# Kernel tuning notes

Hardware: AMD Instinct MI355X
Metric: run time of the kernel (lower is better)

## Reference

```python
import jax, jax.numpy as jnp
import numpy as np

B, D, K, H = 8192, 1024, 8, 2048


def setup_inputs() -> dict:
    key = jax.random.key(0)
    ks = jax.random.split(key, 4)
    x = jax.random.normal(ks[0], (B, D), dtype=jnp.float32)
    centroids = jax.random.normal(ks[1], (K, D), dtype=jnp.float32)
    W1 = jax.random.normal(ks[2], (K, D, H), dtype=jnp.float32) / np.sqrt(D).astype(np.float32)
    b1 = jnp.zeros((K, H), dtype=jnp.float32)
    W2 = jax.random.normal(ks[3], (K, H), dtype=jnp.float32) / np.sqrt(H).astype(np.float32)
    b2 = jnp.zeros((K,), dtype=jnp.float32)
    return {"x": x, "centroids": centroids, "W1": W1, "b1": b1, "W2": W2, "b2": b2}


def reference(x, centroids, W1, b1, W2, b2):
    # --- k-means hard routing: nearest centroid per sample (euclidean max_sim) ---
    # d2[b,k] = ||x_b||^2 - 2 x_b . c_k + ||c_k||^2  (avoid [B,K,D] blowup)
    d2 = (jnp.sum(x * x, axis=-1, keepdims=True)
          - 2.0 * (x @ centroids.T)
          + jnp.sum(centroids * centroids, axis=-1)[None, :])  # [B, K]
    cluster = jnp.argmin(d2, axis=-1)  # [B] int, hard assignment

    # --- per-expert log-likelihood heads (Einet stand-in), computed densely ---
    h = jnp.tanh(jnp.einsum("bd,kdh->kbh", x, W1) + b1[:, None, :])  # [K, B, H]
    lls = jnp.einsum("kbh,kh->kb", h, W2) + b2[:, None]              # [K, B]

    # --- combine: each sample takes the LL from its routed expert, original order ---
    lls_sorted = jnp.take_along_axis(lls.T, cluster[:, None], axis=1)[:, 0]  # [B]
    return lls_sorted
```

## Files before the change

kernel.cpp:

```cpp
#include <hip/hip_runtime.h>
#include <hip/hip_bf16.h>
#include <stdint.h>

#define B_N 8192
#define D_N 1024
#define K_N 8
#define H_N 2048

#define BM 320
#define BN 256
#define BK 64
#define GRID_MT 34
#define ABYTES 40960
#define BUFSZ 73728
#define RO_OFF 147456
#define PLL_OFF 148736
#define GEMM_LDS 153856

typedef unsigned int u32;
typedef unsigned short u16;
typedef __attribute__((ext_vector_type(8))) short short8;
typedef __attribute__((ext_vector_type(4))) float float4v;

struct __align__(8) us4 { u16 x, y, z, w; };

__device__ __forceinline__ u16 f2bf(float f) {
    union { float f; u32 u; } v; v.f = f;
    u32 u = v.u;
    u32 r = (u + 0x7fffu + ((u >> 16) & 1u)) >> 16;
    return (u16)r;
}

__device__ __forceinline__ float fast_tanh(float x) {
    float t = __expf(2.0f * x);
    return 1.0f - 2.0f * __builtin_amdgcn_rcpf(t + 1.0f);
}

__device__ __forceinline__ void async_copy16(void* lds, const void* g) {
    __builtin_amdgcn_global_load_lds(
        (const __attribute__((address_space(1))) void*)g,
        (__attribute__((address_space(3))) void*)lds, 16, 0, 0);
}

__global__ void prep_kernel(const float* __restrict__ w1, u16* __restrict__ w1t,
                            u32* __restrict__ counts,
                            const float* __restrict__ x, const float* __restrict__ cent,
                            const float* __restrict__ b2, u16* __restrict__ xbf,
                            int* __restrict__ cluster, float* __restrict__ out) {
    __shared__ float ts[64][65];
    int tid = threadIdx.x;
    int bid = (int)blockIdx.x;
    int m3 = bid % 3;

    if (m3 == 2) {
        int rb = bid / 3;
        int wave = tid >> 6, lane = tid & 63;
        int b = rb * 4 + wave;
        const float* xr = x + (size_t)b * D_N;

        float4 xv[4];
#pragma unroll
        for (int i = 0; i < 4; ++i)
            xv[i] = *(const float4*)(xr + i * 256 + lane * 4);

#pragma unroll
        for (int i = 0; i < 4; ++i) {
            us4 o;
            o.x = f2bf(xv[i].x); o.y = f2bf(xv[i].y);
            o.z = f2bf(xv[i].z); o.w = f2bf(xv[i].w);
            *(us4*)(xbf + (size_t)b * D_N + i * 256 + lane * 4) = o;
        }

        double acc[K_N];
#pragma unroll
        for (int k = 0; k < K_N; ++k) {
            const float* cr = cent + k * D_N;
            double s = 0.0;
#pragma unroll
            for (int i = 0; i < 4; ++i) {
                float4 cv = *(const float4*)(cr + i * 256 + lane * 4);
                double d0 = (double)xv[i].x - (double)cv.x; s += d0 * d0;
                double d1 = (double)xv[i].y - (double)cv.y; s += d1 * d1;
                double d2 = (double)xv[i].z - (double)cv.z; s += d2 * d2;
                double d3 = (double)xv[i].w - (double)cv.w; s += d3 * d3;
            }
            acc[k] = s;
        }
#pragma unroll
        for (int k = 0; k < K_N; ++k) {
            double v = acc[k];
            for (int off = 32; off; off >>= 1) v += __shfl_down(v, off);
            acc[k] = v;
        }
        if (lane == 0) {
            int best = 0; double bv = acc[0];
#pragma unroll
            for (int k = 1; k < K_N; ++k)
                if (acc[k] < bv) { bv = acc[k]; best = k; }
            cluster[b] = best;
            out[b] = b2[best];
        }
    } else {
        int wi = (bid / 3) * 2 + m3;
        if (wi == 0 && tid < K_N) counts[tid * 32] = 0;
        int hb = wi & 31, db = (wi >> 5) & 15, k = wi >> 9;
        int h0 = hb * 64, d0 = db * 64;
        const float* src = w1 + ((size_t)k * D_N + d0) * H_N + h0;
#pragma unroll
        for (int i = 0; i < 4; ++i) {
            int q = i * 256 + tid;
            int r = q >> 4, c4 = (q & 15) * 4;
            float4 v = *(const float4*)(src + (size_t)r * H_N + c4);
            ts[c4 + 0][r] = v.x; ts[c4 + 1][r] = v.y;
            ts[c4 + 2][r] = v.z; ts[c4 + 3][r] = v.w;
        }
        __syncthreads();
        u16* dst = w1t + ((size_t)k * H_N + h0) * D_N + d0;
#pragma unroll
        for (int i = 0; i < 4; ++i) {
            int q = i * 256 + tid;
            int hr = q >> 4, d4 = (q & 15) * 4;
            us4 o;
            o.x = f2bf(ts[hr][d4 + 0]); o.y = f2bf(ts[hr][d4 + 1]);
            o.z = f2bf(ts[hr][d4 + 2]); o.w = f2bf(ts[hr][d4 + 3]);
            *(us4*)(dst + (size_t)hr * D_N + d4) = o;
        }
    }
}

__global__ void scatter_kernel(const int* __restrict__ cluster,
                               u32* __restrict__ counts,
                               u32* __restrict__ idxl) {
    __shared__ u32 wcnt[4][K_N];
    __shared__ u32 gb[K_N];
    int tid = threadIdx.x;
    int b = blockIdx.x * 256 + tid;
    int lane = tid & 63, wid = tid >> 6;
    int cl = cluster[b];
    unsigned long long lower = (1ull << lane) - 1ull;
    u32 rank = 0;
#pragma unroll
    for (int k = 0; k < K_N; ++k) {
        unsigned long long mk = __ballot(cl == k);
        if (k == cl) rank = (u32)__popcll(mk & lower);
        if (lane == 0) wcnt[wid][k] = (u32)__popcll(mk);
    }
    __syncthreads();
    if (tid < K_N) {
        u32 tot = wcnt[0][tid] + wcnt[1][tid] + wcnt[2][tid] + wcnt[3][tid];
        gb[tid] = atomicAdd(&counts[tid * 32], tot);
    }
    __syncthreads();
    u32 woff = 0;
    if (wid > 0) woff += wcnt[0][cl];
    if (wid > 1) woff += wcnt[1][cl];
    if (wid > 2) woff += wcnt[2][cl];
    idxl[(size_t)cl * B_N + gb[cl] + woff + rank] = (u32)b;
}

__global__ __launch_bounds__(512, 2) void gemm_kernel(
                            const u16* __restrict__ xbf,
                            const u16* __restrict__ w1t,
                            const float* __restrict__ b1,
                            const float* __restrict__ w2,
                            const u32* __restrict__ idxl,
                            const u32* __restrict__ counts,
                            float* __restrict__ out) {
    extern __shared__ char lds[];
    int tix = (int)blockIdx.y;
    int k = -1, mt = 0, ntile = 0;
#pragma unroll
    for (int kk = 0; kk < K_N; ++kk) {
        int c = (int)counts[kk * 32];
        int t = (c + BM - 1) / BM;
        if (tix >= ntile && tix < ntile + t) { k = kk; mt = tix - ntile; }
        ntile += t;
    }
    if (k < 0) return;
    int cnt = (int)counts[k * 32];
    int nc = (int)blockIdx.x;
    int rows = cnt - mt * BM; if (rows > BM) rows = BM;
    int tid = threadIdx.x;
    int lane = tid & 63, w = tid >> 6;
    int wm = w >> 2, wn = w & 3;
    int wmbase = wm * 160;
    int h0 = nc * BN;
    int l15 = lane & 15, l4 = lane >> 4;

    u32* ro = (u32*)(lds + RO_OFF);
    float* pll = (float*)(lds + PLL_OFF);

    if (tid < BM) {
        int m = mt * BM + tid;
        int mm = m < cnt ? m : cnt - 1;
        ro[tid] = idxl[(size_t)k * B_N + mm] * (u32)(D_N * 2);
    }
    __syncthreads();

    u32 srcA[5], srcB[4];
#pragma unroll
    for (int i = 0; i < 5; ++i) {
        int c = i * 512 + tid; int r = c >> 3, j = c & 7;
        srcA[i] = ro[r] + ((u32)(j ^ (r & 7)) << 4);
    }
#pragma unroll
    for (int i = 0; i < 4; ++i) {
        int c = i * 512 + tid; int r = c >> 3, j = c & 7;
        srcB[i] = ((u32)(k * H_N + h0 + r) << 11) + ((u32)(j ^ (r & 7)) << 4);
    }
    const char* xb = (const char*)xbf;
    const char* wb = (const char*)w1t;

    int swz = l15 & 7;
    u32 aB0 = (u32)((wmbase + l15) * 128 + (((0 + l4) ^ swz) << 4));
    u32 aB1 = (u32)((wmbase + l15) * 128 + (((4 + l4) ^ swz) << 4));
    u32 bB0 = (u32)(ABYTES + (wn * 64 + l15) * 128 + (((0 + l4) ^ swz) << 4));
    u32 bB1 = (u32)(ABYTES + (wn * 64 + l15) * 128 + (((4 + l4) ^ swz) << 4));

    float4v acc[10][4];
#pragma unroll
    for (int mf = 0; mf < 10; ++mf)
#pragma unroll
        for (int nf = 0; nf < 4; ++nf)
            acc[mf][nf] = (float4v){0.f, 0.f, 0.f, 0.f};

#define STA(BUF, I, D) async_copy16((BUF) + (I) * 8192 + w * 1024, xb + srcA[I] + (D))
#define STB(BUF, I, D) async_copy16((BUF) + ABYTES + (I) * 8192 + w * 1024, wb + srcB[I] + (D))
#define BAR() do { asm volatile("" ::: "memory"); __builtin_amdgcn_s_barrier(); \
                   asm volatile("" ::: "memory"); } while (0)
#define MFMA_PHASE(MFB, BREG)                                                    \
    do {                                                                         \
        __builtin_amdgcn_s_setprio(1);                                           \
        _Pragma("unroll")                                                        \
        for (int i_ = 0; i_ < 5; ++i_) {                                         \
            if (wmbase + ((MFB) + i_) * 16 < rows) {                             \
                _Pragma("unroll")                                                \
                for (int nf_ = 0; nf_ < 4; ++nf_)                                \
                    acc[(MFB) + i_][nf_] = __builtin_amdgcn_mfma_f32_16x16x32_bf16( \
                        a[i_], BREG[nf_], acc[(MFB) + i_][nf_], 0, 0, 0);        \
            }                                                                    \
        }                                                                        \
        __builtin_amdgcn_s_setprio(0);                                           \
    } while (0)

    {
        char* Bp = lds;
        STA(Bp, 0, 0); STA(Bp, 1, 0); STA(Bp, 2, 0); STA(Bp, 3, 0); STA(Bp, 4, 0);
        STB(Bp, 0, 0); STB(Bp, 1, 0); STB(Bp, 2, 0); STB(Bp, 3, 0);
    }

    for (int t = 0; t < 16; ++t) {
        const char* Acur = lds + (t & 1) * BUFSZ;
        char* Bnx = lds + ((t + 1) & 1) * BUFSZ;
        u32 d = (u32)((t + 1) << 7);
        bool pre = (t < 15);
        short8 a[5], bC[4];

        asm volatile("s_waitcnt vmcnt(0)" ::: "memory");
        BAR();
#pragma unroll
        for (int nf = 0; nf < 4; ++nf)
            bC[nf] = *(const short8*)(Acur + bB0 + nf * 2048);
#pragma unroll
        for (int i = 0; i < 5; ++i)
            a[i] = *(const short8*)(Acur + aB0 + i * 2048);
        if (pre) { STB(Bnx, 0, d); STB(Bnx, 1, d); STB(Bnx, 2, d); }
        BAR();
        MFMA_PHASE(0, bC);

        BAR();
#pragma unroll
        for (int i = 0; i < 5; ++i)
            a[i] = *(const short8*)(Acur + aB0 + (5 + i) * 2048);
        if (pre) { STB(Bnx, 3, d); STA(Bnx, 0, d); STA(Bnx, 1, d); }
        BAR();
        MFMA_PHASE(5, bC);

        BAR();
#pragma unroll
        for (int nf = 0; nf < 4; ++nf)
            bC[nf] = *(const short8*)(Acur + bB1 + nf * 2048);
#pragma unroll
        for (int i = 0; i < 5; ++i)
            a[i] = *(const short8*)(Acur + aB1 + i * 2048);
        if (pre) { STA(Bnx, 2, d); STA(Bnx, 3, d); STA(Bnx, 4, d); }
        BAR();
        MFMA_PHASE(0, bC);

        BAR();
#pragma unroll
        for (int i = 0; i < 5; ++i)
            a[i] = *(const short8*)(Acur + aB1 + (5 + i) * 2048);
        BAR();
        MFMA_PHASE(5, bC);
    }

#undef STA
#undef STB
#undef BAR
#undef MFMA_PHASE

    float w2v[4], b1v[4];
#pragma unroll
    for (int nf = 0; nf < 4; ++nf) {
        int h = h0 + wn * 64 + nf * 16 + l15;
        w2v[nf] = w2[k * H_N + h];
        b1v[nf] = b1[k * H_N + h];
    }
#pragma unroll
    for (int mf = 0; mf < 10; ++mf) {
        float rs[4] = {0.f, 0.f, 0.f, 0.f};
#pragma unroll
        for (int nf = 0; nf < 4; ++nf) {
#pragma unroll
            for (int r = 0; r < 4; ++r)
                rs[r] += fast_tanh(acc[mf][nf][r] + b1v[nf]) * w2v[nf];
        }
#pragma unroll
        for (int r = 0; r < 4; ++r) {
            float v = rs[r];
            v += __shfl_xor(v, 8);
            v += __shfl_xor(v, 4);
            v += __shfl_xor(v, 2);
            v += __shfl_xor(v, 1);
            if (l15 == 0) pll[wn * 320 + wmbase + mf * 16 + l4 * 4 + r] = v;
        }
    }
    __syncthreads();
    if (tid < BM) {
        int m = mt * BM + tid;
        if (m < cnt) {
            u32 b = idxl[(size_t)k * B_N + m];
            atomicAdd(&out[b], pll[tid] + pll[320 + tid] + pll[640 + tid] + pll[960 + tid]);
        }
    }
}

extern "C" void kernel_launch(void* const* d_in, const int* in_sizes, int n_in,
                              void* d_out, int out_size, void* d_ws, size_t ws_size,
                              hipStream_t stream) {
    const float* x    = (const float*)d_in[0];
    const float* cent = (const float*)d_in[1];
    const float* W1   = (const float*)d_in[2];
    const float* b1   = (const float*)d_in[3];
    const float* W2   = (const float*)d_in[4];
    const float* b2   = (const float*)d_in[5];
    float* out = (float*)d_out;

    char* ws = (char*)d_ws;
    u16* xbf     = (u16*)(ws + 0);
    u16* w1t     = (u16*)(ws + 16777216);
    u32* counts  = (u32*)(ws + 50331648);
    int* cluster = (int*)(ws + 50332672);
    u32* idxl    = (u32*)(ws + 50365440);

    (void)hipFuncSetAttribute((const void*)gemm_kernel,
                              hipFuncAttributeMaxDynamicSharedMemorySize, GEMM_LDS);

    hipLaunchKernelGGL(prep_kernel, dim3(6144), dim3(256), 0, stream,
                       W1, w1t, counts, x, cent, b2, xbf, cluster, out);
    hipLaunchKernelGGL(scatter_kernel, dim3(32), dim3(256), 0, stream,
                       cluster, counts, idxl);
    hipLaunchKernelGGL(gemm_kernel, dim3(8, GRID_MT), dim3(512), GEMM_LDS, stream,
                       xbf, w1t, b1, W2, idxl, counts, out);
}
```

Before: 82.06 us.

## Shrink M tile to 256 and split K-step loads into half-stages with partial waits

Reduces the gathered-row GEMM tile from 320 to 256 rows, giving 8 MFMA row fragments per wave instead of 10 and more M tiles (grid 40). The LDS layout changes to split each 64-wide K step into two 32-wide regions with a new swizzle, and the prefetch is issued per half-stage. Waits drop from vmcnt(0) to vmcnt(4), so the second half's loads can still be in flight while the first half computes. This trades some tile-level reuse and extra tile launches for finer-grained overlap, lower register pressure and less LDS.

```diff
diff --git a/kernel.cpp b/kernel.cpp
--- a/kernel.cpp
+++ b/kernel.cpp
@@ -7,15 +7,16 @@
 #define K_N 8
 #define H_N 2048
 
-#define BM 320
+#define BM 256
 #define BN 256
 #define BK 64
-#define GRID_MT 34
-#define ABYTES 40960
-#define BUFSZ 73728
-#define RO_OFF 147456
-#define PLL_OFF 148736
-#define GEMM_LDS 153856
+#define GRID_MT 40
+#define REGB 16384
+#define BUFB 65536
+#define BOFF 32768
+#define RO_OFF 131072
+#define PLL_OFF 132096
+#define GEMM_LDS 136192
 
 typedef unsigned int u32;
 typedef unsigned short u16;
@@ -183,7 +184,7 @@
     int tid = threadIdx.x;
     int lane = tid & 63, w = tid >> 6;
     int wm = w >> 2, wn = w & 3;
-    int wmbase = wm * 160;
+    int wmbase = wm * 128;
     int h0 = nc * BN;
     int l15 = lane & 15, l4 = lane >> 4;
 
@@ -197,42 +198,50 @@
     }
     __syncthreads();
 
-    u32 srcA[5], srcB[4];
-#pragma unroll
-    for (int i = 0; i < 5; ++i) {
-        int c = i * 512 + tid; int r = c >> 3, j = c & 7;
-        srcA[i] = ro[r] + ((u32)(j ^ (r & 7)) << 4);
-    }
-#pragma unroll
-    for (int i = 0; i < 4; ++i) {
-        int c = i * 512 + tid; int r = c >> 3, j = c & 7;
-        srcB[i] = ((u32)(k * H_N + h0 + r) << 11) + ((u32)(j ^ (r & 7)) << 4);
+    u32 srcA[2], srcB[2];
+#pragma unroll
+    for (int i = 0; i < 2; ++i) {
+        int c = i * 512 + tid;
+        int p = c >> 3, u = (c & 7) ^ (p & 7);
+        int row = 2 * p + (u >> 2);
+        srcA[i] = ro[row] + (u32)((u & 3) << 4);
+        srcB[i] = ((u32)(k * H_N + h0 + row) << 11) + (u32)((u & 3) << 4);
     }
     const char* xb = (const char*)xbf;
     const char* wb = (const char*)w1t;
 
-    int swz = l15 & 7;
-    u32 aB0 = (u32)((wmbase + l15) * 128 + (((0 + l4) ^ swz) << 4));
-    u32 aB1 = (u32)((wmbase + l15) * 128 + (((4 + l4) ^ swz) << 4));
-    u32 bB0 = (u32)(ABYTES + (wn * 64 + l15) * 128 + (((0 + l4) ^ swz) << 4));
-    u32 bB1 = (u32)(ABYTES + (wn * 64 + l15) * 128 + (((4 + l4) ^ swz) << 4));
-
-    float4v acc[10][4];
-#pragma unroll
-    for (int mf = 0; mf < 10; ++mf)
+    u32 frOff = (u32)(((l15 >> 1) << 7) |
+                      (((((l15 & 1) << 2) | l4) ^ ((l15 >> 1) & 7)) << 4));
+    u32 aW = (u32)(wmbase * 64) + frOff;
+    u32 bW = (u32)(BOFF + wn * 4096) + frOff;
+
+    float4v acc[8][4];
+#pragma unroll
+    for (int mf = 0; mf < 8; ++mf)
 #pragma unroll
         for (int nf = 0; nf < 4; ++nf)
             acc[mf][nf] = (float4v){0.f, 0.f, 0.f, 0.f};
 
-#define STA(BUF, I, D) async_copy16((BUF) + (I) * 8192 + w * 1024, xb + srcA[I] + (D))
-#define STB(BUF, I, D) async_copy16((BUF) + ABYTES + (I) * 8192 + w * 1024, wb + srcB[I] + (D))
+    auto stA = [&](int tt, int kkh) {
+        char* dst = lds + (tt & 1) * BUFB + kkh * REGB;
+        u32 so = (u32)(kkh * 64 + (tt << 7));
+        async_copy16(dst + tid * 16,        xb + srcA[0] + so);
+        async_copy16(dst + 8192 + tid * 16, xb + srcA[1] + so);
+    };
+    auto stB = [&](int tt, int kkh) {
+        char* dst = lds + (tt & 1) * BUFB + BOFF + kkh * REGB;
+        u32 so = (u32)(kkh * 64 + (tt << 7));
+        async_copy16(dst + tid * 16,        wb + srcB[0] + so);
+        async_copy16(dst + 8192 + tid * 16, wb + srcB[1] + so);
+    };
+
 #define BAR() do { asm volatile("" ::: "memory"); __builtin_amdgcn_s_barrier(); \
                    asm volatile("" ::: "memory"); } while (0)
 #define MFMA_PHASE(MFB, BREG)                                                    \
     do {                                                                         \
         __builtin_amdgcn_s_setprio(1);                                           \
         _Pragma("unroll")                                                        \
-        for (int i_ = 0; i_ < 5; ++i_) {                                         \
+        for (int i_ = 0; i_ < 4; ++i_) {                                         \
             if (wmbase + ((MFB) + i_) * 16 < rows) {                             \
                 _Pragma("unroll")                                                \
                 for (int nf_ = 0; nf_ < 4; ++nf_)                                \
@@ -243,60 +252,55 @@
         __builtin_amdgcn_s_setprio(0);                                           \
     } while (0)
 
-    {
-        char* Bp = lds;
-        STA(Bp, 0, 0); STA(Bp, 1, 0); STA(Bp, 2, 0); STA(Bp, 3, 0); STA(Bp, 4, 0);
-        STB(Bp, 0, 0); STB(Bp, 1, 0); STB(Bp, 2, 0); STB(Bp, 3, 0);
-    }
+    stA(0, 0); stB(0, 0); stA(0, 1); stB(0, 1);
 
     for (int t = 0; t < 16; ++t) {
-        const char* Acur = lds + (t & 1) * BUFSZ;
-        char* Bnx = lds + ((t + 1) & 1) * BUFSZ;
-        u32 d = (u32)((t + 1) << 7);
+        const char* bufc = lds + (t & 1) * BUFB;
         bool pre = (t < 15);
-        short8 a[5], bC[4];
-
-        asm volatile("s_waitcnt vmcnt(0)" ::: "memory");
+        short8 a[4], bC[4];
+
+        asm volatile("s_waitcnt vmcnt(4)" ::: "memory");
         BAR();
 #pragma unroll
         for (int nf = 0; nf < 4; ++nf)
-            bC[nf] = *(const short8*)(Acur + bB0 + nf * 2048);
-#pragma unroll
-        for (int i = 0; i < 5; ++i)
-            a[i] = *(const short8*)(Acur + aB0 + i * 2048);
-        if (pre) { STB(Bnx, 0, d); STB(Bnx, 1, d); STB(Bnx, 2, d); }
+            bC[nf] = *(const short8*)(bufc + bW + nf * 1024);
+#pragma unroll
+        for (int i = 0; i < 4; ++i)
+            a[i] = *(const short8*)(bufc + aW + i * 1024);
+        if (pre) stA(t + 1, 0);
         BAR();
         MFMA_PHASE(0, bC);
 
         BAR();
 #pragma unroll
-        for (int i = 0; i < 5; ++i)
-            a[i] = *(const short8*)(Acur + aB0 + (5 + i) * 2048);
-        if (pre) { STB(Bnx, 3, d); STA(Bnx, 0, d); STA(Bnx, 1, d); }
-        BAR();
-        MFMA_PHASE(5, bC);
-
+        for (int i = 0; i < 4; ++i)
+            a[i] = *(const short8*)(bufc + aW + (4 + i) * 1024);
+        if (pre) stB(t + 1, 0);
+        BAR();
+        MFMA_PHASE(4, bC);
+
+        if (t < 15) asm volatile("s_waitcnt vmcnt(4)" ::: "memory");
+        else        asm volatile("s_waitcnt vmcnt(0)" ::: "memory");
         BAR();
 #pragma unroll
         for (int nf = 0; nf < 4; ++nf)
-            bC[nf] = *(const short8*)(Acur + bB1 + nf * 2048);
-#pragma unroll
-        for (int i = 0; i < 5; ++i)
-            a[i] = *(const short8*)(Acur + aB1 + i * 2048);
-        if (pre) { STA(Bnx, 2, d); STA(Bnx, 3, d); STA(Bnx, 4, d); }
+            bC[nf] = *(const short8*)(bufc + bW + REGB + nf * 1024);
+#pragma unroll
+        for (int i = 0; i < 4; ++i)
+            a[i] = *(const short8*)(bufc + aW + REGB + i * 1024);
+        if (pre) stA(t + 1, 1);
         BAR();
         MFMA_PHASE(0, bC);
 
         BAR();
 #pragma unroll
-        for (int i = 0; i < 5; ++i)
-            a[i] = *(const short8*)(Acur + aB1 + (5 + i) * 2048);
-        BAR();
-        MFMA_PHASE(5, bC);
-    }
-
-#undef STA
-#undef STB
+        for (int i = 0; i < 4; ++i)
+            a[i] = *(const short8*)(bufc + aW + REGB + (4 + i) * 1024);
+        if (pre) stB(t + 1, 1);
+        BAR();
+        MFMA_PHASE(4, bC);
+    }
+
 #undef BAR
 #undef MFMA_PHASE
 
@@ -308,7 +312,7 @@
         b1v[nf] = b1[k * H_N + h];
     }
 #pragma unroll
-    for (int mf = 0; mf < 10; ++mf) {
+    for (int mf = 0; mf < 8; ++mf) {
         float rs[4] = {0.f, 0.f, 0.f, 0.f};
 #pragma unroll
         for (int nf = 0; nf < 4; ++nf) {
@@ -323,7 +327,7 @@
             v += __shfl_xor(v, 4);
             v += __shfl_xor(v, 2);
             v += __shfl_xor(v, 1);
-            if (l15 == 0) pll[wn * 320 + wmbase + mf * 16 + l4 * 4 + r] = v;
+            if (l15 == 0) pll[wn * 256 + wmbase + mf * 16 + l4 * 4 + r] = v;
         }
     }
     __syncthreads();
@@ -331,7 +335,7 @@
         int m = mt * BM + tid;
         if (m < cnt) {
             u32 b = idxl[(size_t)k * B_N + m];
-            atomicAdd(&out[b], pll[tid] + pll[320 + tid] + pll[640 + tid] + pll[960 + tid]);
+            atomicAdd(&out[b], pll[tid] + pll[256 + tid] + pll[512 + tid] + pll[768 + tid]);
         }
     }
 }
```

Result: slower. 105.6 us (+28.7%).
